# Performance work log

Hardware: AMD Instinct MI355X
Metric: run time of the kernel (lower is better)

The kernel has to match this reference:

```python
import jax, jax.numpy as jnp
import numpy as np

B, S, N, F, E, EF, H, L = 4, 16, 2048, 32, 16384, 8, 64, 2
H2 = H // 2


def setup_inputs() -> dict:
    key = jax.random.key(0)
    ks = iter(jax.random.split(key, 40))

    def g(shape, s=0.05):
        return jax.random.normal(next(ks), shape, jnp.float32) * s

    return dict(
        x=jax.random.normal(next(ks), (B, S, N, F), jnp.float32),
        edge_index=jax.random.randint(next(ks), (2, E), 0, N, dtype=jnp.int32),
        edge_attr=jax.random.normal(next(ks), (E, EF), jnp.float32),
        Wp=g((F, H)), bp=jnp.zeros((H,), jnp.float32),
        Wl=g((L, H, H)), bl=jnp.zeros((L, H), jnp.float32),
        Wr=g((L, H, H)), br=jnp.zeros((L, H), jnp.float32),
        We=g((L, EF, H)), att=g((L, H)), gb=jnp.zeros((L, H), jnp.float32),
        Wih=g((L, 3 * H, H)), Whh=g((L, 3 * H, H)),
        bih=jnp.zeros((L, 3 * H), jnp.float32), bhh=jnp.zeros((L, 3 * H), jnp.float32),
        oW1=g((H, H2)), ob1=jnp.zeros((H2,), jnp.float32),
        oW2=g((H2, 1)), ob2=jnp.zeros((1,), jnp.float32),
        dW1=g((H, H2)), db1=jnp.zeros((H2,), jnp.float32),
        dW2=g((H2, 1)), db2=jnp.zeros((1,), jnp.float32),
    )


def reference(x, edge_index, edge_attr, Wp, bp, Wl, bl, Wr, br, We, att, gb,
              Wih, Whh, bih, bhh, oW1, ob1, oW2, ob2, dW1, db1, dW2, db2):
    b, s, n, f = x.shape
    nl, _, h = Wl.shape
    src, dst = edge_index[0], edge_index[1]
    # GATv2Conv add_self_loops with fill_value='mean': self-loop attr = mean of
    # incoming edge attrs per destination node (0 if none).
    ones = jnp.ones((src.shape[0],), x.dtype)
    cnt = jax.ops.segment_sum(ones, dst, num_segments=n)
    loop_attr = jax.ops.segment_sum(edge_attr, dst, num_segments=n) / jnp.maximum(cnt, 1.0)[:, None]
    ar = jnp.arange(n, dtype=src.dtype)
    src_f = jnp.concatenate([src, ar])
    dst_f = jnp.concatenate([dst, ar])
    ea_f = jnp.concatenate([edge_attr, loop_attr], axis=0)  # [E2, EF]

    def gat(Xg, l):
        # Xg: [G, N, H] -- GATv2 (heads=1) applied independently per graph.
        XL = Xg @ Wl[l] + bl[l]
        XR = Xg @ Wr[l] + br[l]
        ep = ea_f @ We[l]                              # [E2, H]
        m = XL[:, src_f] + XR[:, dst_f] + ep[None]     # [G, E2, H]
        m = jax.nn.leaky_relu(m, 0.2)
        logits = m @ att[l]                            # [G, E2]
        seg_max = jax.vmap(lambda lg: jax.ops.segment_max(lg, dst_f, num_segments=n))(logits)
        p = jnp.exp(logits - seg_max[:, dst_f])
        den = jax.vmap(lambda pg: jax.ops.segment_sum(pg, dst_f, num_segments=n))(p)
        alpha = p / den[:, dst_f]
        out = jax.vmap(lambda a, xl: jax.ops.segment_sum(a[:, None] * xl[src_f], dst_f, num_segments=n))(alpha, XL)
        return out + gb[l]

    def gru(seq, l):
        # seq: [T, M, H]; PyTorch GRU gate order (r, z, n), scan over T.
        def step(hprev, xt):
            gi = xt @ Wih[l].T + bih[l]
            gh = hprev @ Whh[l].T + bhh[l]
            ir, iz, inn = jnp.split(gi, 3, -1)
            hr, hz, hn = jnp.split(gh, 3, -1)
            r = jax.nn.sigmoid(ir + hr)
            z = jax.nn.sigmoid(iz + hz)
            nn_ = jnp.tanh(inn + r * hn)
            hnew = (1.0 - z) * nn_ + z * hprev
            return hnew, hnew
        h0 = jnp.zeros(seq.shape[1:], seq.dtype)
        _, ys = jax.lax.scan(step, h0, seq)
        return ys

    X = x @ Wp + bp  # [B, S, N, H]
    for l in range(nl):
        # Original code applies GAT per (outer-t, inner-b) pair; the inner
        # TemporalGNN's GRU recurs over the BATCH axis (length B) per outer t.
        hg = gat(X.reshape(b * s, n, h), l).reshape(b, s, n, h)
        X = gru(hg.reshape(b, s * n, h), l).reshape(b, s, n, h)
    xl = X[:, -1].reshape(b * n, h)  # x[:, -1] then per-node heads, concat dim=1
    order = jax.nn.relu(xl @ oW1 + ob1) @ oW2 + ob2
    demand = jax.nn.relu(xl @ dW1 + db1) @ dW2 + db2
    return order[None], demand[None]  # each [1, B*N, 1]
```

## Files before the change

kernel.cpp:

```cpp
#include <hip/hip_runtime.h>
#include <math.h>

#define Bb   4
#define Ss   16
#define Nn   2048
#define Ff   32
#define Ee   16384
#define EFf  8
#define Hh   64
#define HB2  32
#define E2c  (Ee + Nn)
#define RTOT (Bb*Ss*Nn)
#define Mm   (Ss*Nn)
#define CST  68

typedef __attribute__((ext_vector_type(8))) short short8;
typedef __attribute__((ext_vector_type(4))) float f32x4;
#define MFMA16 __builtin_amdgcn_mfma_f32_16x16x32_bf16

__device__ __forceinline__ float sigf(float x) { return 1.f / (1.f + __expf(-x)); }
__device__ __forceinline__ float tanhfast(float x) { return 2.f / (1.f + __expf(-2.f * x)) - 1.f; }

__device__ __forceinline__ void split_bf16(float x, unsigned short& h, unsigned short& l) {
  unsigned u = __float_as_uint(x);
  unsigned r = (u + 0x7FFFu + ((u >> 16) & 1u)) >> 16;
  h = (unsigned short)r;
  float rest = x - __uint_as_float(r << 16);
  unsigned u2 = __float_as_uint(rest);
  l = (unsigned short)((u2 + 0x7FFFu + ((u2 >> 16) & 1u)) >> 16);
}

template <int PAT>
__device__ __forceinline__ float xorf(float v) {
  return __int_as_float(__builtin_amdgcn_ds_swizzle(__float_as_int(v), PAT));
}
__device__ __forceinline__ float red8(float v) {
  int x = __builtin_amdgcn_update_dpp(0, __float_as_int(v), 0x128, 0xF, 0xF, true);
  v += __int_as_float(x);
  v += xorf<0x401F>(v);
  v += __shfl_xor(v, 32, 64);
  return v;
}
__device__ __forceinline__ float redlogit(float v) {
  int x;
  x = __builtin_amdgcn_update_dpp(0, __float_as_int(v), 0xB1, 0xF, 0xF, true);
  v += __int_as_float(x);
  x = __builtin_amdgcn_update_dpp(0, __float_as_int(v), 0x4E, 0xF, 0xF, true);
  v += __int_as_float(x);
  v += xorf<0x101F>(v);
  return v;
}

__global__ __launch_bounds__(256) void k_loop_accum(
    const int* __restrict__ ei, const float* __restrict__ ea,
    float* __restrict__ cntF, float* __restrict__ loopA) {
  int idx = blockIdx.x * 256 + threadIdx.x;
  int e = idx >> 3, j = idx & 7;
  int d = ei[Ee + e];
  atomicAdd(&loopA[d * EFf + j], ea[idx]);
  if (j == 0) atomicAdd(&cntF[d], 1.0f);
}

__global__ __launch_bounds__(256) void k_scan(
    const float* __restrict__ cntF, int* __restrict__ offs) {
  __shared__ int partial[256];
  int tid = threadIdx.x;
  int base = tid * 8;
  int vals[8];
  int s = 0;
  for (int i = 0; i < 8; ++i) {
    int c = (int)cntF[base + i] + 1;
    vals[i] = c;
    s += c;
  }
  partial[tid] = s;
  __syncthreads();
  for (int off = 1; off < 256; off <<= 1) {
    int v = partial[tid];
    int add = (tid >= off) ? partial[tid - off] : 0;
    __syncthreads();
    partial[tid] = v + add;
    __syncthreads();
  }
  int run = (tid == 0) ? 0 : partial[tid - 1];
  for (int i = 0; i < 8; ++i) {
    offs[base + i] = run;
    run += vals[i];
  }
  if (tid == 255) offs[Nn] = run;
}

__global__ __launch_bounds__(256) void k_scatter(
    const int* __restrict__ ei, const int* __restrict__ offs,
    int* __restrict__ fillI, int* __restrict__ posOf, int* __restrict__ srcA) {
  int e = blockIdx.x * 256 + threadIdx.x;
  if (e >= E2c) return;
  int d = (e < Ee) ? ei[Ee + e] : (e - Ee);
  int s = (e < Ee) ? ei[e]      : (e - Ee);
  int pos = offs[d] + atomicAdd(&fillI[d], 1);
  posOf[e] = pos;
  srcA[pos] = s;
}

__global__ __launch_bounds__(256) void k_wprep(
    const float* __restrict__ Wl, const float* __restrict__ Wr,
    const float* __restrict__ Wih, const float* __restrict__ Whh,
    unsigned short* __restrict__ WXhi, unsigned short* __restrict__ WXlo,
    unsigned short* __restrict__ WGhi, unsigned short* __restrict__ WGlo) {
  int idx = blockIdx.x * 256 + threadIdx.x;
  if (idx < 16384) {
    int j = idx & 7, lane = (idx >> 3) & 63, kh = (idx >> 9) & 1;
    int t = (idx >> 10) & 7, l = idx >> 13;
    int n = t * 16 + (lane & 15);
    int k = kh * 32 + ((lane >> 4) << 3) + j;
    const float* W = (n < 64) ? (Wl + (size_t)l * 4096) : (Wr + (size_t)l * 4096);
    float v = W[k * 64 + (n & 63)];
    unsigned short h, lo;
    split_bf16(v, h, lo);
    WXhi[idx] = h; WXlo[idx] = lo;
  } else {
    int i2 = idx - 16384;
    int j = i2 & 7, lane = (i2 >> 3) & 63, kh = (i2 >> 9) & 1;
    int t = (i2 >> 10) % 24, l = i2 / 24576;
    int n = t * 16 + (lane & 15);
    int k = kh * 32 + ((lane >> 4) << 3) + j;
    int g = n >> 6, c = n & 63;
    const float* W = (g < 3) ? (Wih + (size_t)l * 12288 + (size_t)(g * 64 + c) * 64)
                             : (Whh + (size_t)l * 12288 + (size_t)((g - 3) * 64 + c) * 64);
    float v = W[k];
    unsigned short h, lo;
    split_bf16(v, h, lo);
    WGhi[i2] = h; WGlo[i2] = lo;
  }
}

__global__ __launch_bounds__(256) void k_ep(
    const float* __restrict__ ea, const float* __restrict__ loopA,
    const float* __restrict__ We, const int* __restrict__ posOf,
    const float* __restrict__ cntF, float* __restrict__ EPc) {
  __shared__ float wlds[EFf * Hh];
  int tid = threadIdx.x;
  int l = blockIdx.y;
  const float* Wel = We + (size_t)l * EFf * Hh;
  if (tid < EFf * Hh) wlds[tid] = Wel[tid];
  if (tid + 256 < EFf * Hh) wlds[tid + 256] = Wel[tid + 256];
  __syncthreads();
  int idx = blockIdx.x * 256 + tid;
  int e = idx >> 6, j = idx & 63;
  const float* a = (e < Ee) ? (ea + (size_t)e * EFf) : (loopA + (size_t)(e - Ee) * EFf);
  float acc = 0.f;
#pragma unroll
  for (int k = 0; k < EFf; ++k) acc += a[k] * wlds[k * Hh + j];
  if (e >= Ee) acc /= fmaxf(cntF[e - Ee], 1.0f);
  EPc[(size_t)l * E2c * Hh + (((size_t)posOf[e]) << 6) + j] = acc;
}

__global__ __launch_bounds__(256) void k_proj(
    const float* __restrict__ X, const float* __restrict__ Wp,
    const float* __restrict__ bp, float* __restrict__ Out) {
  __shared__ float w[32 * 16];
  int tid = threadIdx.x;
  int j0 = blockIdx.y << 4;
  for (int idx = tid; idx < 32 * 16; idx += 256)
    w[idx] = Wp[((idx >> 4) << 6) + j0 + (idx & 15)];
  __syncthreads();
  int r0 = (blockIdx.x << 9) + tid;
  float acc[2][16];
#pragma unroll
  for (int jj = 0; jj < 16; ++jj) { float b = bp[j0 + jj]; acc[0][jj] = b; acc[1][jj] = b; }
  const float* x0 = X + ((size_t)r0 << 5);
  const float* x1 = x0 + (256 << 5);
  for (int kc = 0; kc < 8; ++kc) {
    float4 a0 = *(const float4*)(x0 + 4 * kc);
    float4 a1 = *(const float4*)(x1 + 4 * kc);
    float a0a[4] = {a0.x, a0.y, a0.z, a0.w};
    float a1a[4] = {a1.x, a1.y, a1.z, a1.w};
#pragma unroll
    for (int q = 0; q < 4; ++q) {
      const float4* wp4 = (const float4*)(w + ((4 * kc + q) << 4));
#pragma unroll
      for (int q4 = 0; q4 < 4; ++q4) {
        float4 wv = wp4[q4];
        acc[0][4*q4+0] = fmaf(a0a[q], wv.x, acc[0][4*q4+0]);
        acc[0][4*q4+1] = fmaf(a0a[q], wv.y, acc[0][4*q4+1]);
        acc[0][4*q4+2] = fmaf(a0a[q], wv.z, acc[0][4*q4+2]);
        acc[0][4*q4+3] = fmaf(a0a[q], wv.w, acc[0][4*q4+3]);
        acc[1][4*q4+0] = fmaf(a1a[q], wv.x, acc[1][4*q4+0]);
        acc[1][4*q4+1] = fmaf(a1a[q], wv.y, acc[1][4*q4+1]);
        acc[1][4*q4+2] = fmaf(a1a[q], wv.z, acc[1][4*q4+2]);
        acc[1][4*q4+3] = fmaf(a1a[q], wv.w, acc[1][4*q4+3]);
      }
    }
  }
#pragma unroll
  for (int rr = 0; rr < 2; ++rr) {
    float* op = Out + (((size_t)(r0 + 256 * rr)) << 6) + j0;
#pragma unroll
    for (int q4 = 0; q4 < 4; ++q4)
      *(float4*)(op + 4 * q4) = make_float4(acc[rr][4*q4], acc[rr][4*q4+1], acc[rr][4*q4+2], acc[rr][4*q4+3]);
  }
}

__global__ __launch_bounds__(256) void k_xlr_mm(
    const float* __restrict__ X,
    const unsigned short* __restrict__ WXhi, const unsigned short* __restrict__ WXlo,
    const float* __restrict__ bl_, const float* __restrict__ br_,
    float* __restrict__ XL, float* __restrict__ XR) {
  __shared__ unsigned short ahi[4096], alo[4096];
  __shared__ float cbuf[64 * CST];
  int tid = threadIdx.x, lane = tid & 63, wv = tid >> 6;
  size_t m0 = (size_t)blockIdx.x << 6;
#pragma unroll
  for (int it = 0; it < 2; ++it) {
    int task = (it << 8) + tid;
    int row = task >> 3, cOct = task & 7;
    const float* src = X + ((m0 + row) << 6) + (cOct << 3);
    float4 a = *(const float4*)src;
    float4 b = *(const float4*)(src + 4);
    float va[8] = {a.x, a.y, a.z, a.w, b.x, b.y, b.z, b.w};
    short8 hv, lv;
#pragma unroll
    for (int j = 0; j < 8; ++j) {
      unsigned short hs, ls;
      split_bf16(va[j], hs, ls);
      hv[j] = (short)hs; lv[j] = (short)ls;
    }
    int f = ((cOct >> 2) * 4 + (row >> 4)) * 64 + ((cOct & 3) << 4) + (row & 15);
    *(short8*)&ahi[f << 3] = hv;
    *(short8*)&alo[f << 3] = lv;
  }
  __syncthreads();
  short8 Ah0 = *(const short8*)&ahi[((0 + wv) << 6 | lane) << 3];
  short8 Al0 = *(const short8*)&alo[((0 + wv) << 6 | lane) << 3];
  short8 Ah1 = *(const short8*)&ahi[((4 + wv) << 6 | lane) << 3];
  short8 Al1 = *(const short8*)&alo[((4 + wv) << 6 | lane) << 3];
  int nl = lane & 15;
  f32x4 acc[8];
#pragma unroll
  for (int t = 0; t < 8; ++t) {
    int n = t * 16 + nl;
    float b = (n < 64) ? bl_[n] : br_[n - 64];
    acc[t] = (f32x4){b, b, b, b};
  }
#pragma unroll
  for (int t = 0; t < 8; ++t) {
    const short8* bh0p = (const short8*)(WXhi + ((t << 1) << 9)) + lane;
    const short8* bl0p = (const short8*)(WXlo + ((t << 1) << 9)) + lane;
    const short8* bh1p = (const short8*)(WXhi + (((t << 1) + 1) << 9)) + lane;
    const short8* bl1p = (const short8*)(WXlo + (((t << 1) + 1) << 9)) + lane;
    short8 bh0 = *bh0p, bl0 = *bl0p, bh1 = *bh1p, bl1 = *bl1p;
    acc[t] = MFMA16(Ah0, bh0, acc[t], 0, 0, 0);
    acc[t] = MFMA16(Ah0, bl0, acc[t], 0, 0, 0);
    acc[t] = MFMA16(Al0, bh0, acc[t], 0, 0, 0);
    acc[t] = MFMA16(Ah1, bh1, acc[t], 0, 0, 0);
    acc[t] = MFMA16(Ah1, bl1, acc[t], 0, 0, 0);
    acc[t] = MFMA16(Al1, bh1, acc[t], 0, 0, 0);
  }
  int rbase = (wv << 4) + ((lane >> 4) << 2);
#pragma unroll
  for (int half = 0; half < 2; ++half) {
    __syncthreads();
#pragma unroll
    for (int tt = 0; tt < 4; ++tt) {
      int t = (half << 2) + tt;
#pragma unroll
      for (int reg = 0; reg < 4; ++reg)
        cbuf[(rbase + reg) * CST + (tt << 4) + nl] = acc[t][reg];
    }
    __syncthreads();
    float* dst = half ? XR : XL;
#pragma unroll
    for (int i = 0; i < 4; ++i) {
      int idx = (i << 10) + (tid << 2);
      int row = idx >> 6, col = idx & 63;
      *(float4*)(dst + ((m0 + row) << 6) + col) = *(float4*)&cbuf[row * CST + col];
    }
  }
}

__global__ __launch_bounds__(256) void k_gat(
    const float* __restrict__ XL, float* __restrict__ XR_HG,
    const float* __restrict__ EPc, const int* __restrict__ offs,
    const int* __restrict__ srcA,
    const float* __restrict__ att, const float* __restrict__ gbl) {
  int d = blockIdx.x;
  int q = blockIdx.y;
  int tid = threadIdx.x;
  int wv = tid >> 6, lane = tid & 63;
  int eSub = lane >> 3, hOct = lane & 7;
  int hb = hOct << 3;
  float at[8], gv[8];
  {
    float4 a0 = *(const float4*)(att + hb);
    float4 a1 = *(const float4*)(att + hb + 4);
    float4 g0v = *(const float4*)(gbl + hb);
    float4 g1v = *(const float4*)(gbl + hb + 4);
    at[0]=a0.x; at[1]=a0.y; at[2]=a0.z; at[3]=a0.w;
    at[4]=a1.x; at[5]=a1.y; at[6]=a1.z; at[7]=a1.w;
    gv[0]=g0v.x; gv[1]=g0v.y; gv[2]=g0v.z; gv[3]=g0v.w;
    gv[4]=g1v.x; gv[5]=g1v.y; gv[6]=g1v.z; gv[7]=g1v.w;
  }
  int p0 = offs[d], p1 = offs[d + 1];
  int nE = p1 - p0;
  int nCh = (nE + 7) >> 3;
  int gbase = (q << 4) + wv;
  size_t rowg[4];
  const float* Xg[4];
  float xr[4][8];
#pragma unroll
  for (int c = 0; c < 4; ++c) {
    int g = gbase + (c << 2);
    rowg[c] = ((size_t)(g * Nn + d)) << 6;
    Xg[c] = XL + (((size_t)g * Nn) << 6);
    float4 a = *(const float4*)(XR_HG + rowg[c] + hb);
    float4 b = *(const float4*)(XR_HG + rowg[c] + hb + 4);
    xr[c][0]=a.x; xr[c][1]=a.y; xr[c][2]=a.z; xr[c][3]=a.w;
    xr[c][4]=b.x; xr[c][5]=b.y; xr[c][6]=b.z; xr[c][7]=b.w;
  }
  float Sd[4] = {0.f, 0.f, 0.f, 0.f};
  float acc[4][8];
#pragma unroll
  for (int c = 0; c < 4; ++c)
#pragma unroll
    for (int j = 0; j < 8; ++j) acc[c][j] = 0.f;

  for (int ck = 0; ck < nCh; ++ck) {
    int p = (ck << 3) + eSub;
    int pc = p < nE ? p : nE - 1;
    int s = srcA[p0 + pc];
    const float* epp = EPc + (((size_t)(p0 + pc)) << 6) + hb;
    float4 e0 = *(const float4*)epp;
    float4 e1 = *(const float4*)(epp + 4);
    float ep[8] = {e0.x, e0.y, e0.z, e0.w, e1.x, e1.y, e1.z, e1.w};
    float xlv[4][8];
#pragma unroll
    for (int c = 0; c < 4; ++c) {
      const float* xp = Xg[c] + ((size_t)s << 6) + hb;
      float4 x0 = *(const float4*)xp;
      float4 x1 = *(const float4*)(xp + 4);
      xlv[c][0]=x0.x; xlv[c][1]=x0.y; xlv[c][2]=x0.z; xlv[c][3]=x0.w;
      xlv[c][4]=x1.x; xlv[c][5]=x1.y; xlv[c][6]=x1.z; xlv[c][7]=x1.w;
    }
    float v[4] = {0.f, 0.f, 0.f, 0.f};
#pragma unroll
    for (int c = 0; c < 4; ++c)
#pragma unroll
      for (int j = 0; j < 8; ++j) {
        float m = xlv[c][j] + xr[c][j] + ep[j];
        m = fmaxf(m, 0.2f * m);
        v[c] = fmaf(m, at[j], v[c]);
      }
#pragma unroll
    for (int c = 0; c < 4; ++c) v[c] = redlogit(v[c]);
    bool live = (p < nE);
#pragma unroll
    for (int c = 0; c < 4; ++c) {
      float w = live ? __expf(v[c]) : 0.f;
      Sd[c] += w;
#pragma unroll
      for (int j = 0; j < 8; ++j) acc[c][j] = fmaf(w, xlv[c][j], acc[c][j]);
    }
  }
#pragma unroll
  for (int c = 0; c < 4; ++c) {
    Sd[c] = red8(Sd[c]);
#pragma unroll
    for (int j = 0; j < 8; ++j) acc[c][j] = red8(acc[c][j]);
  }
  if (eSub == 0) {
#pragma unroll
    for (int c = 0; c < 4; ++c) {
      float inv = 1.f / Sd[c];
      float* op = XR_HG + rowg[c] + hb;
      *(float4*)(op)     = make_float4(fmaf(acc[c][0], inv, gv[0]), fmaf(acc[c][1], inv, gv[1]),
                                       fmaf(acc[c][2], inv, gv[2]), fmaf(acc[c][3], inv, gv[3]));
      *(float4*)(op + 4) = make_float4(fmaf(acc[c][4], inv, gv[4]), fmaf(acc[c][5], inv, gv[5]),
                                       fmaf(acc[c][6], inv, gv[6]), fmaf(acc[c][7], inv, gv[7]));
    }
  }
}

__device__ __forceinline__ void mm6r(f32x4& acc,
    short8 Ah0, short8 Al0, short8 Ah1, short8 Al1,
    short8 bh0, short8 bl0, short8 bh1, short8 bl1) {
  acc = MFMA16(Ah0, bh0, acc, 0, 0, 0);
  acc = MFMA16(Ah0, bl0, acc, 0, 0, 0);
  acc = MFMA16(Al0, bh0, acc, 0, 0, 0);
  acc = MFMA16(Ah1, bh1, acc, 0, 0, 0);
  acc = MFMA16(Ah1, bl1, acc, 0, 0, 0);
  acc = MFMA16(Al1, bh1, acc, 0, 0, 0);
}

template <int SLICE>
__global__ __launch_bounds__(256, 2) void k_gru_fused(
    const float* __restrict__ hgAll,
    const unsigned short* __restrict__ WGhi, const unsigned short* __restrict__ WGlo,
    const float* __restrict__ bih, const float* __restrict__ bhh,
    float* __restrict__ houtAll) {
  __shared__ unsigned short ghi[4096], glo[4096];
  __shared__ float cbuf[64 * CST];
  int tid = threadIdx.x, lane = tid & 63, wv = tid >> 6;
  int nl = lane & 15;
  int rb0 = (lane >> 4) << 2;
  size_t m0 = (size_t)blockIdx.x << 6;

  short8 Wh[6][2], Wl[6][2];
#pragma unroll
  for (int g = 0; g < 6; ++g) {
    int tt = wv + (g << 2);
    Wh[g][0] = *((const short8*)(WGhi + (tt << 10)) + lane);
    Wh[g][1] = *((const short8*)(WGhi + (tt << 10) + 512) + lane);
    Wl[g][0] = *((const short8*)(WGlo + (tt << 10)) + lane);
    Wl[g][1] = *((const short8*)(WGlo + (tt << 10) + 512) + lane);
  }

  float biasR, biasZ, biasN, biasH;
  {
    int c = (wv << 4) + nl;
    biasR = bih[c]       + bhh[c];
    biasZ = bih[64 + c]  + bhh[64 + c];
    biasN = bih[128 + c];
    biasH = bhh[128 + c];
  }

  float4 pa[2], pb[2];
#pragma unroll
  for (int it = 0; it < 2; ++it) {
    int task = (it << 8) + tid;
    int row = task >> 3, cOct = task & 7;
    const float* srcg = hgAll + ((m0 + row) << 6) + (cOct << 3);
    pa[it] = *(const float4*)srcg;
    pb[it] = *(const float4*)(srcg + 4);
  }

  for (int t = 0; t < Bb; ++t) {
#pragma unroll
    for (int it = 0; it < 2; ++it) {
      int task = (it << 8) + tid;
      int row = task >> 3, cOct = task & 7;
      float va[8] = {pa[it].x, pa[it].y, pa[it].z, pa[it].w,
                     pb[it].x, pb[it].y, pb[it].z, pb[it].w};
      short8 hv8, lv8;
#pragma unroll
      for (int j = 0; j < 8; ++j) {
        unsigned short hs, ls;
        split_bf16(va[j], hs, ls);
        hv8[j] = (short)hs; lv8[j] = (short)ls;
      }
      int f = ((cOct >> 2) * 4 + (row >> 4)) * 64 + ((cOct & 3) << 4) + (row & 15);
      *(short8*)&ghi[f << 3] = hv8;
      *(short8*)&glo[f << 3] = lv8;
    }
    __syncthreads();

    if (t + 1 < Bb) {
      const float* hg = hgAll + (size_t)(t + 1) * ((size_t)Mm * Hh);
#pragma unroll
      for (int it = 0; it < 2; ++it) {
        int task = (it << 8) + tid;
        int row = task >> 3, cOct = task & 7;
        const float* srcg = hg + ((m0 + row) << 6) + (cOct << 3);
        pa[it] = *(const float4*)srcg;
        pb[it] = *(const float4*)(srcg + 4);
      }
    }

    f32x4 accR[4], accZ[4], accN[4], accH[4];
#pragma unroll
    for (int rg = 0; rg < 4; ++rg) {
      accR[rg] = (f32x4){biasR, biasR, biasR, biasR};
      accZ[rg] = (f32x4){biasZ, biasZ, biasZ, biasZ};
      accN[rg] = (f32x4){biasN, biasN, biasN, biasN};
      accH[rg] = (f32x4){biasH, biasH, biasH, biasH};
    }
#pragma unroll
    for (int rg = 0; rg < 4; ++rg) {
      short8 Gh0 = *(const short8*)&ghi[((0 + rg) << 6 | lane) << 3];
      short8 Gl0 = *(const short8*)&glo[((0 + rg) << 6 | lane) << 3];
      short8 Gh1 = *(const short8*)&ghi[((4 + rg) << 6 | lane) << 3];
      short8 Gl1 = *(const short8*)&glo[((4 + rg) << 6 | lane) << 3];
      mm6r(accR[rg], Gh0, Gl0, Gh1, Gl1, Wh[0][0], Wl[0][0], Wh[0][1], Wl[0][1]);
      mm6r(accZ[rg], Gh0, Gl0, Gh1, Gl1, Wh[1][0], Wl[1][0], Wh[1][1], Wl[1][1]);
      mm6r(accN[rg], Gh0, Gl0, Gh1, Gl1, Wh[2][0], Wl[2][0], Wh[2][1], Wl[2][1]);
      if (t) {
        const float* cb = &cbuf[((rg << 4) + (lane & 15)) * CST + ((lane >> 4) << 3)];
        float4 p00 = *(const float4*)cb;
        float4 p01 = *(const float4*)(cb + 4);
        float4 p10 = *(const float4*)(cb + 32);
        float4 p11 = *(const float4*)(cb + 36);
        float v0[8] = {p00.x, p00.y, p00.z, p00.w, p01.x, p01.y, p01.z, p01.w};
        float v1[8] = {p10.x, p10.y, p10.z, p10.w, p11.x, p11.y, p11.z, p11.w};
        short8 Ph0, Pl0, Ph1, Pl1;
#pragma unroll
        for (int j = 0; j < 8; ++j) {
          unsigned short hs, ls;
          split_bf16(v0[j], hs, ls);
          Ph0[j] = (short)hs; Pl0[j] = (short)ls;
          split_bf16(v1[j], hs, ls);
          Ph1[j] = (short)hs; Pl1[j] = (short)ls;
        }
        mm6r(accR[rg], Ph0, Pl0, Ph1, Pl1, Wh[3][0], Wl[3][0], Wh[3][1], Wl[3][1]);
        mm6r(accZ[rg], Ph0, Pl0, Ph1, Pl1, Wh[4][0], Wl[4][0], Wh[4][1], Wl[4][1]);
        mm6r(accH[rg], Ph0, Pl0, Ph1, Pl1, Wh[5][0], Wl[5][0], Wh[5][1], Wl[5][1]);
      }
    }
    __syncthreads();

#pragma unroll
    for (int rg = 0; rg < 4; ++rg) {
#pragma unroll
      for (int r = 0; r < 4; ++r) {
        float rgate = sigf(accR[rg][r]);
        float zg = sigf(accZ[rg][r]);
        float ng = tanhfast(accN[rg][r] + rgate * accH[rg][r]);
        int ci = ((rg << 4) + rb0 + r) * CST + (wv << 4) + nl;
        float hp = t ? cbuf[ci] : 0.f;
        cbuf[ci] = (1.f - zg) * ng + zg * hp;
      }
    }
    __syncthreads();

    if (SLICE == 0 || blockIdx.x >= (Mm / 64 - Nn / 64)) {
      float* hout = houtAll + (size_t)t * ((size_t)Mm * Hh);
#pragma unroll
      for (int i = 0; i < 4; ++i) {
        int idx = (i << 10) + (tid << 2);
        int row = idx >> 6, col = idx & 63;
        *(float4*)(hout + ((m0 + row) << 6) + col) = *(float4*)&cbuf[row * CST + col];
      }
    }
  }
}

__global__ __launch_bounds__(256) void k_heads(
    const float* __restrict__ Xb,
    const float* __restrict__ oW1, const float* __restrict__ ob1,
    const float* __restrict__ oW2, const float* __restrict__ ob2,
    const float* __restrict__ dW1, const float* __restrict__ db1,
    const float* __restrict__ dW2, const float* __restrict__ db2,
    float* __restrict__ out) {
  __shared__ float xa[64 * 65];
  __shared__ float w1o[64 * 32], w1d[64 * 32];
  __shared__ float po[4][64], pd[4][64];
  int tid = threadIdx.x;
  int rblk = blockIdx.x << 6;
  int b = rblk >> 11;
  int n0 = rblk & (Nn - 1);
  const float* src = Xb + (((size_t)b * Ss + (Ss - 1)) * Nn + n0) * Hh;
#pragma unroll
  for (int i = 0; i < 4; ++i) {
    int idx = (i << 10) + (tid << 2);
    int row = idx >> 6, col = idx & 63;
    float4 v = *(const float4*)(src + idx);
    float* dp = &xa[row * 65 + col];
    dp[0] = v.x; dp[1] = v.y; dp[2] = v.z; dp[3] = v.w;
  }
  for (int idx = tid; idx < 2048; idx += 256) {
    w1o[idx] = oW1[idx];
    w1d[idx] = dW1[idx];
  }
  __syncthreads();
  int row = tid & 63;
  int jg = tid >> 6;
  int j0 = jg << 3;
  float hO[8], hD[8];
#pragma unroll
  for (int j = 0; j < 8; ++j) { hO[j] = ob1[j0 + j]; hD[j] = db1[j0 + j]; }
  const float* xr = &xa[row * 65];
  for (int k = 0; k < 64; ++k) {
    float xv = xr[k];
    const float4* wo = (const float4*)&w1o[(k << 5) + j0];
    const float4* wd = (const float4*)&w1d[(k << 5) + j0];
    float4 o0 = wo[0], o1 = wo[1], d0 = wd[0], d1 = wd[1];
    hO[0] = fmaf(xv, o0.x, hO[0]); hO[1] = fmaf(xv, o0.y, hO[1]);
    hO[2] = fmaf(xv, o0.z, hO[2]); hO[3] = fmaf(xv, o0.w, hO[3]);
    hO[4] = fmaf(xv, o1.x, hO[4]); hO[5] = fmaf(xv, o1.y, hO[5]);
    hO[6] = fmaf(xv, o1.z, hO[6]); hO[7] = fmaf(xv, o1.w, hO[7]);
    hD[0] = fmaf(xv, d0.x, hD[0]); hD[1] = fmaf(xv, d0.y, hD[1]);
    hD[2] = fmaf(xv, d0.z, hD[2]); hD[3] = fmaf(xv, d0.w, hD[3]);
    hD[4] = fmaf(xv, d1.x, hD[4]); hD[5] = fmaf(xv, d1.y, hD[5]);
    hD[6] = fmaf(xv, d1.z, hD[6]); hD[7] = fmaf(xv, d1.w, hD[7]);
  }
  float accoP = 0.f, accdP = 0.f;
#pragma unroll
  for (int j = 0; j < 8; ++j) {
    accoP = fmaf(fmaxf(hO[j], 0.f), oW2[j0 + j], accoP);
    accdP = fmaf(fmaxf(hD[j], 0.f), dW2[j0 + j], accdP);
  }
  po[jg][row] = accoP;
  pd[jg][row] = accdP;
  __syncthreads();
  if (tid < 64) {
    int r = rblk + tid;
    out[r]           = ob2[0] + ((po[0][tid] + po[1][tid]) + (po[2][tid] + po[3][tid]));
    out[Bb * Nn + r] = db2[0] + ((pd[0][tid] + pd[1][tid]) + (pd[2][tid] + pd[3][tid]));
  }
}

extern "C" void kernel_launch(void* const* d_in, const int* in_sizes, int n_in,
                              void* d_out, int out_size, void* d_ws, size_t ws_size,
                              hipStream_t stream) {
  const float* x   = (const float*)d_in[0];
  const int*   ei  = (const int*)d_in[1];
  const float* ea  = (const float*)d_in[2];
  const float* Wp  = (const float*)d_in[3];
  const float* bp  = (const float*)d_in[4];
  const float* Wl  = (const float*)d_in[5];
  const float* bl  = (const float*)d_in[6];
  const float* Wr  = (const float*)d_in[7];
  const float* br  = (const float*)d_in[8];
  const float* We  = (const float*)d_in[9];
  const float* att = (const float*)d_in[10];
  const float* gb  = (const float*)d_in[11];
  const float* Wih = (const float*)d_in[12];
  const float* Whh = (const float*)d_in[13];
  const float* bih = (const float*)d_in[14];
  const float* bhh = (const float*)d_in[15];
  const float* oW1 = (const float*)d_in[16];
  const float* ob1 = (const float*)d_in[17];
  const float* oW2 = (const float*)d_in[18];
  const float* ob2 = (const float*)d_in[19];
  const float* dW1 = (const float*)d_in[20];
  const float* db1 = (const float*)d_in[21];
  const float* dW2 = (const float*)d_in[22];
  const float* db2 = (const float*)d_in[23];
  float* out = (float*)d_out;

  float* f    = (float*)d_ws;
  float* Xb   = f;
  float* XLb  = Xb  + (size_t)RTOT * Hh;
  float* XRb  = XLb + (size_t)RTOT * Hh;
  float* EPc  = XRb + (size_t)RTOT * Hh;
  unsigned short* WXhi = (unsigned short*)(EPc + (size_t)2 * E2c * Hh);
  unsigned short* WXlo = WXhi + 16384;
  unsigned short* WGhi = WXlo + 16384;
  unsigned short* WGlo = WGhi + 49152;
  float* cntF = (float*)(WGlo + 49152);
  float* loopA = cntF + Nn;
  int*   fillI = (int*)(loopA + Nn * EFf);
  int*   offs  = fillI + Nn;
  int*   posOf = offs + 2052;
  int*   srcA  = posOf + E2c;

  hipMemsetAsync(cntF, 0, (size_t)(Nn + Nn * EFf + Nn) * 4, stream);

  k_loop_accum<<<dim3(Ee * EFf / 256), 256, 0, stream>>>(ei, ea, cntF, loopA);
  k_scan<<<1, 256, 0, stream>>>(cntF, offs);
  k_scatter<<<dim3((E2c + 255) / 256), 256, 0, stream>>>(ei, offs, fillI, posOf, srcA);
  k_wprep<<<dim3(256), 256, 0, stream>>>(Wl, Wr, Wih, Whh, WXhi, WXlo, WGhi, WGlo);

  k_proj<<<dim3(RTOT / 512, 4), 256, 0, stream>>>(x, Wp, bp, Xb);

  k_ep<<<dim3(E2c * Hh / 256, 2), 256, 0, stream>>>(ea, loopA, We, posOf, cntF, EPc);

  for (int l = 0; l < 2; ++l) {
    k_xlr_mm<<<dim3(RTOT / 64), 256, 0, stream>>>(
        Xb, WXhi + (size_t)l * 8192, WXlo + (size_t)l * 8192,
        bl + (size_t)l * Hh, br + (size_t)l * Hh, XLb, XRb);
    k_gat<<<dim3(Nn, 4), 256, 0, stream>>>(
        XLb, XRb, EPc + (size_t)l * E2c * Hh, offs, srcA,
        att + (size_t)l * Hh, gb + (size_t)l * Hh);
    if (l == 0) {
      k_gru_fused<0><<<dim3(Mm / 64), 256, 0, stream>>>(
          XRb, WGhi, WGlo, bih, bhh, Xb);
    } else {
      k_gru_fused<1><<<dim3(Mm / 64), 256, 0, stream>>>(
          XRb, WGhi + (size_t)24576, WGlo + (size_t)24576,
          bih + (size_t)192, bhh + (size_t)192, Xb);
    }
  }

  k_heads<<<dim3(Bb * Nn / 64), 256, 0, stream>>>(
      Xb, oW1, ob1, oW2, ob2, dW1, db1, dW2, db2, out);
}
```

Measured before the change: 377.6 us.

## Fuse layer-1 XL/XR projection into layer-0 GRU kernel epilogue

Adds a kernel that runs the layer-0 GRU recurrence and, at each step, projects the new hidden state through the layer-1 Wl/Wr weights, writing XL and XR directly. This removes the second k_xlr_mm launch and its round trip of the full hidden state through global memory. In exchange the GRU kernel does extra MFMA work and streams the projection weights from global memory every step, adds more barriers, and overwrites its input buffer in place, which assumes each block reads only its own rows.

```diff
diff --git a/kernel.cpp b/kernel.cpp
--- a/kernel.cpp
+++ b/kernel.cpp
@@ -391,6 +391,192 @@
   acc = MFMA16(Al1, bh1, acc, 0, 0, 0);
 }
 
+__global__ __launch_bounds__(256, 2) void k_gru_xlr(
+    float* xrbuf,
+    const unsigned short* __restrict__ WGhi, const unsigned short* __restrict__ WGlo,
+    const float* __restrict__ bih, const float* __restrict__ bhh,
+    const unsigned short* __restrict__ WXhi, const unsigned short* __restrict__ WXlo,
+    const float* __restrict__ bl_, const float* __restrict__ br_,
+    float* __restrict__ XL) {
+  __shared__ unsigned short ghi[4096], glo[4096];
+  __shared__ float cbuf[64 * CST];
+  int tid = threadIdx.x, lane = tid & 63, wv = tid >> 6;
+  int nl = lane & 15;
+  int rb0 = (lane >> 4) << 2;
+  size_t m0 = (size_t)blockIdx.x << 6;
+
+  short8 Wh[6][2], Wl[6][2];
+#pragma unroll
+  for (int g = 0; g < 6; ++g) {
+    int tt = wv + (g << 2);
+    Wh[g][0] = *((const short8*)(WGhi + (tt << 10)) + lane);
+    Wh[g][1] = *((const short8*)(WGhi + (tt << 10) + 512) + lane);
+    Wl[g][0] = *((const short8*)(WGlo + (tt << 10)) + lane);
+    Wl[g][1] = *((const short8*)(WGlo + (tt << 10) + 512) + lane);
+  }
+
+  float biasR, biasZ, biasN, biasH;
+  {
+    int c = (wv << 4) + nl;
+    biasR = bih[c]       + bhh[c];
+    biasZ = bih[64 + c]  + bhh[64 + c];
+    biasN = bih[128 + c];
+    biasH = bhh[128 + c];
+  }
+
+  float4 pa[2], pb[2];
+#pragma unroll
+  for (int it = 0; it < 2; ++it) {
+    int task = (it << 8) + tid;
+    int row = task >> 3, cOct = task & 7;
+    const float* srcg = xrbuf + ((m0 + row) << 6) + (cOct << 3);
+    pa[it] = *(const float4*)srcg;
+    pb[it] = *(const float4*)(srcg + 4);
+  }
+
+  for (int t = 0; t < Bb; ++t) {
+#pragma unroll
+    for (int it = 0; it < 2; ++it) {
+      int task = (it << 8) + tid;
+      int row = task >> 3, cOct = task & 7;
+      float va[8] = {pa[it].x, pa[it].y, pa[it].z, pa[it].w,
+                     pb[it].x, pb[it].y, pb[it].z, pb[it].w};
+      short8 hv8, lv8;
+#pragma unroll
+      for (int j = 0; j < 8; ++j) {
+        unsigned short hs, ls;
+        split_bf16(va[j], hs, ls);
+        hv8[j] = (short)hs; lv8[j] = (short)ls;
+      }
+      int f = ((cOct >> 2) * 4 + (row >> 4)) * 64 + ((cOct & 3) << 4) + (row & 15);
+      *(short8*)&ghi[f << 3] = hv8;
+      *(short8*)&glo[f << 3] = lv8;
+    }
+    __syncthreads();
+
+    if (t + 1 < Bb) {
+      const float* hg = xrbuf + (size_t)(t + 1) * ((size_t)Mm * Hh);
+#pragma unroll
+      for (int it = 0; it < 2; ++it) {
+        int task = (it << 8) + tid;
+        int row = task >> 3, cOct = task & 7;
+        const float* srcg = hg + ((m0 + row) << 6) + (cOct << 3);
+        pa[it] = *(const float4*)srcg;
+        pb[it] = *(const float4*)(srcg + 4);
+      }
+    }
+
+    f32x4 accR[4], accZ[4], accN[4], accH[4];
+#pragma unroll
+    for (int rg = 0; rg < 4; ++rg) {
+      accR[rg] = (f32x4){biasR, biasR, biasR, biasR};
+      accZ[rg] = (f32x4){biasZ, biasZ, biasZ, biasZ};
+      accN[rg] = (f32x4){biasN, biasN, biasN, biasN};
+      accH[rg] = (f32x4){biasH, biasH, biasH, biasH};
+    }
+#pragma unroll
+    for (int rg = 0; rg < 4; ++rg) {
+      short8 Gh0 = *(const short8*)&ghi[((0 + rg) << 6 | lane) << 3];
+      short8 Gl0 = *(const short8*)&glo[((0 + rg) << 6 | lane) << 3];
+      short8 Gh1 = *(const short8*)&ghi[((4 + rg) << 6 | lane) << 3];
+      short8 Gl1 = *(const short8*)&glo[((4 + rg) << 6 | lane) << 3];
+      mm6r(accR[rg], Gh0, Gl0, Gh1, Gl1, Wh[0][0], Wl[0][0], Wh[0][1], Wl[0][1]);
+      mm6r(accZ[rg], Gh0, Gl0, Gh1, Gl1, Wh[1][0], Wl[1][0], Wh[1][1], Wl[1][1]);
+      mm6r(accN[rg], Gh0, Gl0, Gh1, Gl1, Wh[2][0], Wl[2][0], Wh[2][1], Wl[2][1]);
+      if (t) {
+        const float* cb = &cbuf[((rg << 4) + (lane & 15)) * CST + ((lane >> 4) << 3)];
+        float4 p00 = *(const float4*)cb;
+        float4 p01 = *(const float4*)(cb + 4);
+        float4 p10 = *(const float4*)(cb + 32);
+        float4 p11 = *(const float4*)(cb + 36);
+        float v0[8] = {p00.x, p00.y, p00.z, p00.w, p01.x, p01.y, p01.z, p01.w};
+        float v1[8] = {p10.x, p10.y, p10.z, p10.w, p11.x, p11.y, p11.z, p11.w};
+        short8 Ph0, Pl0, Ph1, Pl1;
+#pragma unroll
+        for (int j = 0; j < 8; ++j) {
+          unsigned short hs, ls;
+          split_bf16(v0[j], hs, ls);
+          Ph0[j] = (short)hs; Pl0[j] = (short)ls;
+          split_bf16(v1[j], hs, ls);
+          Ph1[j] = (short)hs; Pl1[j] = (short)ls;
+        }
+        mm6r(accR[rg], Ph0, Pl0, Ph1, Pl1, Wh[3][0], Wl[3][0], Wh[3][1], Wl[3][1]);
+        mm6r(accZ[rg], Ph0, Pl0, Ph1, Pl1, Wh[4][0], Wl[4][0], Wh[4][1], Wl[4][1]);
+        mm6r(accH[rg], Ph0, Pl0, Ph1, Pl1, Wh[5][0], Wl[5][0], Wh[5][1], Wl[5][1]);
+      }
+    }
+    __syncthreads();
+
+#pragma unroll
+    for (int rg = 0; rg < 4; ++rg) {
+#pragma unroll
+      for (int r = 0; r < 4; ++r) {
+        float rgate = sigf(accR[rg][r]);
+        float zg = sigf(accZ[rg][r]);
+        float ng = tanhfast(accN[rg][r] + rgate * accH[rg][r]);
+        int ci = ((rg << 4) + rb0 + r) * CST + (wv << 4) + nl;
+        float hp = t ? cbuf[ci] : 0.f;
+        cbuf[ci] = (1.f - zg) * ng + zg * hp;
+      }
+    }
+    __syncthreads();
+
+#pragma unroll
+    for (int it = 0; it < 2; ++it) {
+      int task = (it << 8) + tid;
+      int row = task >> 3, cOct = task & 7;
+      const float* srcp = &cbuf[row * CST + (cOct << 3)];
+      float4 a = *(const float4*)srcp;
+      float4 b = *(const float4*)(srcp + 4);
+      float va[8] = {a.x, a.y, a.z, a.w, b.x, b.y, b.z, b.w};
+      short8 hv8, lv8;
+#pragma unroll
+      for (int j = 0; j < 8; ++j) {
+        unsigned short hs, ls;
+        split_bf16(va[j], hs, ls);
+        hv8[j] = (short)hs; lv8[j] = (short)ls;
+      }
+      int f = ((cOct >> 2) * 4 + (row >> 4)) * 64 + ((cOct & 3) << 4) + (row & 15);
+      *(short8*)&ghi[f << 3] = hv8;
+      *(short8*)&glo[f << 3] = lv8;
+    }
+    __syncthreads();
+
+    short8 Ah0 = *(const short8*)&ghi[((0 + wv) << 6 | lane) << 3];
+    short8 Al0 = *(const short8*)&glo[((0 + wv) << 6 | lane) << 3];
+    short8 Ah1 = *(const short8*)&ghi[((4 + wv) << 6 | lane) << 3];
+    short8 Al1 = *(const short8*)&glo[((4 + wv) << 6 | lane) << 3];
+    __syncthreads();
+
+    f32x4 xacc[8];
+#pragma unroll
+    for (int t8 = 0; t8 < 8; ++t8) {
+      int n = t8 * 16 + nl;
+      float b = (n < 64) ? bl_[n] : br_[n - 64];
+      xacc[t8] = (f32x4){b, b, b, b};
+    }
+#pragma unroll
+    for (int t8 = 0; t8 < 8; ++t8) {
+      const short8* bh0p = (const short8*)(WXhi + ((t8 << 1) << 9)) + lane;
+      const short8* bl0p = (const short8*)(WXlo + ((t8 << 1) << 9)) + lane;
+      const short8* bh1p = (const short8*)(WXhi + (((t8 << 1) + 1) << 9)) + lane;
+      const short8* bl1p = (const short8*)(WXlo + (((t8 << 1) + 1) << 9)) + lane;
+      short8 bh0 = *bh0p, bl0 = *bl0p, bh1 = *bh1p, bl1 = *bl1p;
+      mm6r(xacc[t8], Ah0, Al0, Ah1, Al1, bh0, bl0, bh1, bl1);
+    }
+
+    size_t grow = (size_t)t * Mm + m0 + (wv << 4) + rb0;
+#pragma unroll
+    for (int t8 = 0; t8 < 8; ++t8) {
+      float* dst = (t8 < 4) ? XL : xrbuf;
+      int col = ((t8 & 3) << 4) + nl;
+#pragma unroll
+      for (int r = 0; r < 4; ++r)
+        dst[((grow + r) << 6) + col] = xacc[t8][r];
+    }
+  }
+}
+
 template <int SLICE>
 __global__ __launch_bounds__(256, 2) void k_gru_fused(
     const float* __restrict__ hgAll,
@@ -653,22 +839,19 @@
 
   k_ep<<<dim3(E2c * Hh / 256, 2), 256, 0, stream>>>(ea, loopA, We, posOf, cntF, EPc);
 
-  for (int l = 0; l < 2; ++l) {
-    k_xlr_mm<<<dim3(RTOT / 64), 256, 0, stream>>>(
-        Xb, WXhi + (size_t)l * 8192, WXlo + (size_t)l * 8192,
-        bl + (size_t)l * Hh, br + (size_t)l * Hh, XLb, XRb);
-    k_gat<<<dim3(Nn, 4), 256, 0, stream>>>(
-        XLb, XRb, EPc + (size_t)l * E2c * Hh, offs, srcA,
-        att + (size_t)l * Hh, gb + (size_t)l * Hh);
-    if (l == 0) {
-      k_gru_fused<0><<<dim3(Mm / 64), 256, 0, stream>>>(
-          XRb, WGhi, WGlo, bih, bhh, Xb);
-    } else {
-      k_gru_fused<1><<<dim3(Mm / 64), 256, 0, stream>>>(
-          XRb, WGhi + (size_t)24576, WGlo + (size_t)24576,
-          bih + (size_t)192, bhh + (size_t)192, Xb);
-    }
-  }
+  k_xlr_mm<<<dim3(RTOT / 64), 256, 0, stream>>>(
+      Xb, WXhi, WXlo, bl, br, XLb, XRb);
+  k_gat<<<dim3(Nn, 4), 256, 0, stream>>>(
+      XLb, XRb, EPc, offs, srcA, att, gb);
+  k_gru_xlr<<<dim3(Mm / 64), 256, 0, stream>>>(
+      XRb, WGhi, WGlo, bih, bhh,
+      WXhi + 8192, WXlo + 8192, bl + 64, br + 64, XLb);
+
+  k_gat<<<dim3(Nn, 4), 256, 0, stream>>>(
+      XLb, XRb, EPc + (size_t)E2c * Hh, offs, srcA,
+      att + 64, gb + 64);
+  k_gru_fused<1><<<dim3(Mm / 64), 256, 0, stream>>>(
+      XRb, WGhi + 24576, WGlo + 24576, bih + 192, bhh + 192, Xb);
 
   k_heads<<<dim3(Bb * Nn / 64), 256, 0, stream>>>(
       Xb, oW1, ob1, oW2, ob2, dW1, db1, dW2, db2, out);
```

Result: slower. 430.9 us (+14.1%).
